# Kernel optimization log

Measured on AMD Instinct MI355X. Metric: run time of the kernel, lower is better.

## Reference

```python
import jax, jax.numpy as jnp
import numpy as np

B, S, D, H = 2, 2048, 2048, 16
HD = D // H


def setup_inputs() -> dict:
    key = jax.random.key(0)
    kx, = jax.random.split(key, 1)
    return {
        "x": jax.random.normal(kx, (B, S, D), dtype=jnp.float32),
        "q_mask": jnp.ones((D, D), dtype=jnp.float32),
        "k_mask": jnp.ones((D, D), dtype=jnp.float32),
        "v_mask": jnp.ones((D, D), dtype=jnp.float32),
        "out_mask": jnp.ones((D, D), dtype=jnp.float32),
        "head_mask": jnp.ones((H,), dtype=jnp.float32),
        "attention_mask": jnp.ones((B, S), dtype=jnp.float32),
        "shared_weight": jnp.float32(1.0),
    }


def reference(x, q_mask, k_mask, v_mask, out_mask, head_mask, attention_mask, shared_weight):
    b, s, d = x.shape
    scale = jnp.float32(HD) ** -0.5

    def shared_linear(inp, mask):
        # F.linear(x, mask * shared_weight): out = inp @ (mask*sw).T
        return jnp.einsum("bsd,ed->bse", inp, mask * shared_weight)

    q = shared_linear(x, q_mask).reshape(b, s, H, HD).transpose(0, 2, 1, 3)  # [B,H,S,HD]
    k = shared_linear(x, k_mask).reshape(b, s, H, HD).transpose(0, 2, 1, 3)
    v = shared_linear(x, v_mask).reshape(b, s, H, HD).transpose(0, 2, 1, 3)

    hm = head_mask.reshape(1, H, 1, 1)
    q, k, v = q * hm, k * hm, v * hm

    scores = jnp.einsum("bhqd,bhkd->bhqk", q, k) * scale  # [B,H,S,S]

    # causal mask: upper triangle (j > i) -> -inf
    causal = jnp.triu(jnp.ones((s, s), dtype=bool), k=1)
    scores = jnp.where(causal, -jnp.inf, scores)

    # additive attention mask: (1 - m) * -10000, broadcast [B,1,1,S]
    scores = scores + (1.0 - attention_mask)[:, None, None, :] * -10000.0

    attn = jax.nn.softmax(scores, axis=-1)  # dropout is identity in eval / p=0

    out = jnp.einsum("bhqk,bhkd->bhqd", attn, v)          # [B,H,S,HD]
    out = out.transpose(0, 2, 1, 3).reshape(b, s, d)       # [B,S,D]
    return shared_linear(out, out_mask)
```

## Files before the change

kernel.cpp:

```cpp
#include <hip/hip_runtime.h>

#define B_  2
#define S_  2048
#define D_  2048
#define H_  16
#define HD_ 128

typedef __bf16 bf16;
typedef __bf16 bf16x4 __attribute__((ext_vector_type(4)));
typedef __bf16 bf16x8 __attribute__((ext_vector_type(8)));
typedef float  f32x4  __attribute__((ext_vector_type(4)));

__device__ __forceinline__ void gld_lds16(const void* g, void* l) {
    __builtin_amdgcn_global_load_lds(
        (const __attribute__((address_space(1))) unsigned int*)g,
        (__attribute__((address_space(3))) unsigned int*)l, 16, 0, 0);
}

__global__ __launch_bounds__(256)
void precast_kernel(const float* __restrict__ x, bf16* __restrict__ xh,
                    bf16* __restrict__ xl) {
    int i = (blockIdx.x * 256 + threadIdx.x) * 8;
    float4 a = *(const float4*)(x + i);
    float4 b = *(const float4*)(x + i + 4);
    float av[8] = {a.x, a.y, a.z, a.w, b.x, b.y, b.z, b.w};
    bf16x8 h8, l8;
#pragma unroll
    for (int e = 0; e < 8; e++) {
        bf16 hv = (bf16)av[e];
        h8[e] = hv;
        l8[e] = (bf16)(av[e] - (float)hv);
    }
    *(bf16x8*)(xh + i) = h8;
    *(bf16x8*)(xl + i) = l8;
}

__global__ __launch_bounds__(256)
void transpose_v(const bf16* __restrict__ vp, bf16* __restrict__ vt) {
    const int bh = blockIdx.x >> 5;
    const int s0 = (blockIdx.x & 31) * 64;
    const int t = threadIdx.x;
    __shared__ bf16 tile[128 * 72];
    const bf16* src = vp + (size_t)bh * S_ * HD_;
    bf16* dst = vt + (size_t)bh * HD_ * S_;

    {
        int r = t >> 2;
        int g = (t & 3) * 4;
#pragma unroll
        for (int w = 0; w < 4; w++) {
            bf16x8 v8 = *(const bf16x8*)&src[(size_t)(s0 + r) * HD_ + (g + w) * 8];
#pragma unroll
            for (int e = 0; e < 8; e++) tile[((g + w) * 8 + e) * 72 + r] = v8[e];
        }
    }
    __syncthreads();
    {
        int d = t >> 1;
        int sg0 = (t & 1) * 4;
#pragma unroll
        for (int w = 0; w < 4; w++) {
            int sg = sg0 + w;
            *(bf16x8*)&dst[(size_t)d * S_ + s0 + sg * 8] =
                *(const bf16x8*)&tile[d * 72 + sg * 8];
        }
    }
}

#define BK 64

template<int MODE>
__global__ __launch_bounds__(256, 3)
void gemm_nt(const bf16* __restrict__ Ah_g, const bf16* __restrict__ Al_g,
             const float* __restrict__ B0, const float* __restrict__ B1,
             const float* __restrict__ B2,
             const float* __restrict__ swp, const float* __restrict__ hm,
             bf16* __restrict__ qh_, bf16* __restrict__ ql_,
             bf16* __restrict__ kh_, bf16* __restrict__ kl_,
             bf16* __restrict__ vp_, float* __restrict__ Cf) {
    const int K = D_;
    __shared__ bf16 Ah[128 * 64];
    __shared__ bf16 Al[128 * 64];
    __shared__ bf16 Bs[128 * 64];
    const int t = threadIdx.x;
    const int wave = t >> 6, lane = t & 63;
    const int wr = wave >> 1, wc = wave & 1;
    const int m0 = blockIdx.y * 128, n0 = blockIdx.x * 128;
    const int lrow = lane & 15, lquad = lane >> 4;
    const float sw = swp[0];

    const int which = (MODE == 0) ? (n0 >> 11) : 0;
    const bool split = (MODE == 0) && (which < 2);

    const float* Bp;
    if (MODE == 0) {
        Bp = (which == 0) ? B0 : ((which == 1) ? B1 : B2);
        Bp += (size_t)(n0 & (D_ - 1)) * K;
    } else {
        Bp = B0 + (size_t)n0 * K;
    }

    const int srow8 = lane >> 3;
    const int sgrp  = lane & 7;
    const int g0 = (lquad)     ^ (lrow & 7);
    const int g1 = (lquad + 4) ^ (lrow & 7);

    f32x4 acc[4][4];
#pragma unroll
    for (int i = 0; i < 4; i++)
#pragma unroll
        for (int j = 0; j < 4; j++) acc[i][j] = (f32x4){0.f, 0.f, 0.f, 0.f};

    for (int k0 = 0; k0 < K; k0 += BK) {
#pragma unroll
        for (int p = 0; p < 4; p++) {
            int r = wave * 32 + p * 8 + srow8;
            int gcol = (sgrp ^ (r & 7)) * 8;
            gld_lds16(Ah_g + (size_t)(m0 + r) * K + k0 + gcol,
                      &Ah[(wave * 32 + p * 8) * 64]);
            if (split)
                gld_lds16(Al_g + (size_t)(m0 + r) * K + k0 + gcol,
                          &Al[(wave * 32 + p * 8) * 64]);
        }
#pragma unroll
        for (int p = 0; p < 4; p++) {
            int r = p * 32 + (t >> 3);
            int gcol = (sgrp ^ (r & 7)) * 8;
            const float* bp = Bp + (size_t)r * K + k0 + gcol;
            float4 blo = *(const float4*)bp;
            float4 bhi = *(const float4*)(bp + 4);
            bf16x8 b8;
            b8[0] = (bf16)(blo.x * sw); b8[1] = (bf16)(blo.y * sw);
            b8[2] = (bf16)(blo.z * sw); b8[3] = (bf16)(blo.w * sw);
            b8[4] = (bf16)(bhi.x * sw); b8[5] = (bf16)(bhi.y * sw);
            b8[6] = (bf16)(bhi.z * sw); b8[7] = (bf16)(bhi.w * sw);
            *(bf16x8*)&Bs[r * 64 + sgrp * 8] = b8;
        }
        __syncthreads();

#pragma unroll
        for (int kk = 0; kk < 2; kk++) {
            const int gA = kk ? g1 : g0;
            bf16x8 afh[4], afl[4], bfr[4];
#pragma unroll
            for (int i = 0; i < 4; i++) {
                int row = wr * 64 + i * 16 + lrow;
                afh[i] = *(const bf16x8*)&Ah[row * 64 + gA * 8];
                if (split) afl[i] = *(const bf16x8*)&Al[row * 64 + gA * 8];
            }
#pragma unroll
            for (int j = 0; j < 4; j++) {
                int row = wc * 64 + j * 16 + lrow;
                bfr[j] = *(const bf16x8*)&Bs[row * 64 + gA * 8];
            }
#pragma unroll
            for (int i = 0; i < 4; i++)
#pragma unroll
                for (int j = 0; j < 4; j++) {
                    acc[i][j] = __builtin_amdgcn_mfma_f32_16x16x32_bf16(
                        afh[i], bfr[j], acc[i][j], 0, 0, 0);
                    if (split)
                        acc[i][j] = __builtin_amdgcn_mfma_f32_16x16x32_bf16(
                            afl[i], bfr[j], acc[i][j], 0, 0, 0);
                }
        }
        __syncthreads();
    }

#pragma unroll
    for (int i = 0; i < 4; i++) {
#pragma unroll
        for (int j = 0; j < 4; j++) {
#pragma unroll
            for (int r = 0; r < 4; r++) {
                int m = m0 + wr * 64 + i * 16 + lquad * 4 + r;
                int n = n0 + wc * 64 + j * 16 + lrow;
                float v = acc[i][j][r];
                if (MODE == 0) {
                    int e = n & (D_ - 1);
                    int h = e >> 7, hd = e & (HD_ - 1);
                    int b = m >> 11, s = m & (S_ - 1);
                    v *= hm[h];
                    size_t idx = (((size_t)b * H_ + h) * S_ + s) * HD_ + hd;
                    if (which == 2) {
                        vp_[idx] = (bf16)v;
                    } else {
                        bf16 hv = (bf16)v;
                        bf16 lv = (bf16)(v - (float)hv);
                        if (which == 0) { qh_[idx] = hv; ql_[idx] = lv; }
                        else            { kh_[idx] = hv; kl_[idx] = lv; }
                    }
                } else {
                    Cf[(size_t)m * D_ + n] = v;
                }
            }
        }
    }
}

#define SPLD 72

__global__ __launch_bounds__(256, 2)
void attn_kernel(const bf16* __restrict__ qh_, const bf16* __restrict__ ql_,
                 const bf16* __restrict__ kh_, const bf16* __restrict__ kl_,
                 const bf16* __restrict__ vt_, const float* __restrict__ am,
                 bf16* __restrict__ outp) {
    const int bh = blockIdx.x & 31;
    const int qblk = 31 - (blockIdx.x >> 5);
    const int b = bh >> 4, h = bh & 15;
    const int i0 = qblk * 64;
    const int t = threadIdx.x, wave = t >> 6, lane = t & 63;
    const int lrow = lane & 15, quad = lane >> 4;

    __shared__ bf16 skh[64 * 128];
    __shared__ bf16 skl[64 * 128];
    __shared__ bf16 svt[128 * 64];
    __shared__ bf16 sp[4][16 * SPLD];

    const size_t kbase = (size_t)bh * S_ * HD_;
    const size_t vbase = (size_t)bh * HD_ * S_;

    const int qrow = i0 + wave * 16 + lrow;
    bf16x8 qhf[4], qlf[4];
#pragma unroll
    for (int c = 0; c < 4; c++) {
        qhf[c] = *(const bf16x8*)&qh_[kbase + (size_t)qrow * HD_ + c * 32 + quad * 8];
        qlf[c] = *(const bf16x8*)&ql_[kbase + (size_t)qrow * HD_ + c * 32 + quad * 8];
    }

    float m_i[4], l_i[4];
    f32x4 O[8];
#pragma unroll
    for (int r = 0; r < 4; r++) { m_i[r] = -INFINITY; l_i[r] = 0.f; }
#pragma unroll
    for (int n2 = 0; n2 < 8; n2++) O[n2] = (f32x4){0.f, 0.f, 0.f, 0.f};

    const float scale = 0.08838834764831845f;

    for (int j0 = 0; j0 <= i0; j0 += 64) {
        __syncthreads();
#pragma unroll
        for (int p = 0; p < 4; p++) {
            int rb = wave * 16 + p * 4;
            int r = rb + (lane >> 4);
            int gl = ((lane & 15) ^ (r & 7)) * 8;
            gld_lds16(kh_ + kbase + (size_t)(j0 + r) * HD_ + gl, &skh[rb * 128]);
            gld_lds16(kl_ + kbase + (size_t)(j0 + r) * HD_ + gl, &skl[rb * 128]);
        }
#pragma unroll
        for (int p = 0; p < 4; p++) {
            int db = wave * 32 + p * 8;
            int d = db + (lane >> 3);
            int gl = ((lane & 7) ^ (d & 7)) * 8;
            gld_lds16(vt_ + vbase + (size_t)d * S_ + j0 + gl, &svt[db * 64]);
        }
        __syncthreads();

        float amadd[4];
#pragma unroll
        for (int nt = 0; nt < 4; nt++)
            amadd[nt] = (1.0f - am[b * S_ + j0 + nt * 16 + lrow]) * -10000.0f;

        f32x4 s4[4];
#pragma unroll
        for (int nt = 0; nt < 4; nt++) s4[nt] = (f32x4){0.f, 0.f, 0.f, 0.f};
#pragma unroll
        for (int c = 0; c < 4; c++) {
#pragma unroll
            for (int nt = 0; nt < 4; nt++) {
                int ka = (nt * 16 + lrow) * 128 + (((c * 4 + quad) ^ (lrow & 7)) * 8);
                bf16x8 kb8 = *(const bf16x8*)&skh[ka];
                bf16x8 lb8 = *(const bf16x8*)&skl[ka];
                s4[nt] = __builtin_amdgcn_mfma_f32_16x16x32_bf16(qhf[c], kb8, s4[nt], 0, 0, 0);
                s4[nt] = __builtin_amdgcn_mfma_f32_16x16x32_bf16(qhf[c], lb8, s4[nt], 0, 0, 0);
                s4[nt] = __builtin_amdgcn_mfma_f32_16x16x32_bf16(qlf[c], kb8, s4[nt], 0, 0, 0);
            }
        }

        const bool diag = (j0 == i0);
#pragma unroll
        for (int r = 0; r < 4; r++) {
            const int rrow = wave * 16 + quad * 4 + r;
            float sv[4], pw[4];
            float mx = -INFINITY;
#pragma unroll
            for (int nt = 0; nt < 4; nt++) {
                float xv = s4[nt][r] * scale + amadd[nt];
                if (diag && (nt * 16 + lrow) > rrow) xv = -INFINITY;
                sv[nt] = xv;
                mx = fmaxf(mx, xv);
            }
#pragma unroll
            for (int off = 1; off < 16; off <<= 1) mx = fmaxf(mx, __shfl_xor(mx, off));
            float mnew = fmaxf(m_i[r], mx);
            float alpha = __expf(m_i[r] - mnew);
            float ps = 0.f;
#pragma unroll
            for (int nt = 0; nt < 4; nt++) { pw[nt] = __expf(sv[nt] - mnew); ps += pw[nt]; }
#pragma unroll
            for (int off = 1; off < 16; off <<= 1) ps += __shfl_xor(ps, off);
            l_i[r] = l_i[r] * alpha + ps;
            m_i[r] = mnew;
#pragma unroll
            for (int n2 = 0; n2 < 8; n2++) O[n2][r] *= alpha;
#pragma unroll
            for (int nt = 0; nt < 4; nt++)
                sp[wave][(quad * 4 + r) * SPLD + nt * 16 + lrow] = (bf16)pw[nt];
        }
        __asm__ volatile("s_waitcnt lgkmcnt(0)" ::: "memory");

#pragma unroll
        for (int k2 = 0; k2 < 2; k2++) {
            bf16x8 pf = *(const bf16x8*)&sp[wave][lrow * SPLD + k2 * 32 + quad * 8];
            const int gp = ((quad + k2 * 4) ^ (lrow & 7)) * 8;
#pragma unroll
            for (int n2 = 0; n2 < 8; n2++) {
                bf16x8 vf8 = *(const bf16x8*)&svt[(n2 * 16 + lrow) * 64 + gp];
                O[n2] = __builtin_amdgcn_mfma_f32_16x16x32_bf16(pf, vf8, O[n2], 0, 0, 0);
            }
        }
    }

    float inv[4];
#pragma unroll
    for (int r = 0; r < 4; r++) inv[r] = 1.0f / l_i[r];
#pragma unroll
    for (int n2 = 0; n2 < 8; n2++)
#pragma unroll
        for (int r = 0; r < 4; r++) {
            int srow = i0 + wave * 16 + quad * 4 + r;
            outp[((size_t)(b * S_ + srow)) * D_ + h * HD_ + n2 * 16 + lrow] =
                (bf16)(O[n2][r] * inv[r]);
        }
}

extern "C" void kernel_launch(void* const* d_in, const int* in_sizes, int n_in,
                              void* d_out, int out_size, void* d_ws, size_t ws_size,
                              hipStream_t stream) {
    const float* x  = (const float*)d_in[0];
    const float* qm = (const float*)d_in[1];
    const float* km = (const float*)d_in[2];
    const float* vm = (const float*)d_in[3];
    const float* om = (const float*)d_in[4];
    const float* hm = (const float*)d_in[5];
    const float* am = (const float*)d_in[6];
    const float* sw = (const float*)d_in[7];
    float* out = (float*)d_out;

    const size_t P = (size_t)B_ * H_ * S_ * HD_ * sizeof(bf16);
    char* ws = (char*)d_ws;
    bf16* xh = (bf16*)(ws + 0 * P);
    bf16* xl = (bf16*)(ws + 1 * P);
    bf16* qh = (bf16*)(ws + 2 * P);
    bf16* ql = (bf16*)(ws + 3 * P);
    bf16* kh = (bf16*)(ws + 4 * P);
    bf16* kl = (bf16*)(ws + 5 * P);
    bf16* vp = (bf16*)d_out;
    bf16* vt = (bf16*)((char*)d_out + P);
    bf16* attn_out = (bf16*)(ws + 0 * P);

    precast_kernel<<<(B_ * S_ * D_) / (256 * 8), 256, 0, stream>>>(x, xh, xl);

    gemm_nt<0><<<dim3(48, 32), 256, 0, stream>>>(
        xh, xl, qm, km, vm, sw, hm, qh, ql, kh, kl, vp, nullptr);

    transpose_v<<<1024, 256, 0, stream>>>(vp, vt);

    attn_kernel<<<1024, 256, 0, stream>>>(qh, ql, kh, kl, vt, am, attn_out);

    gemm_nt<1><<<dim3(16, 32), 256, 0, stream>>>(
        attn_out, nullptr, om, nullptr, nullptr, sw, hm,
        nullptr, nullptr, nullptr, nullptr, nullptr, out);
}
```

Baseline: 493.7 us.

## Double-buffer 32-key attention tiles with prefetch and per-wave causal skipping

The attention loop now works on 32-key chunks held in double-buffered LDS, issuing async global-to-LDS loads for the next chunk before computing the current one, so only one barrier is needed per iteration. Each wave skips chunks lying entirely above its own causal diagonal. The row-sum of probabilities moves from a shuffle reduction to an extra MFMA against a ones vector. LDS drops to one shared buffer and launch bounds rise to 3 blocks per CU for occupancy, at the cost of more loop iterations and a tighter register budget.

Measured after the change: 496.7 us. No clear change (+0.6%).

```diff
diff --git a/kernel.cpp b/kernel.cpp
--- a/kernel.cpp
+++ b/kernel.cpp
@@ -43,7 +43,6 @@
     __shared__ bf16 tile[128 * 72];
     const bf16* src = vp + (size_t)bh * S_ * HD_;
     bf16* dst = vt + (size_t)bh * HD_ * S_;
-
     {
         int r = t >> 2;
         int g = (t & 3) * 4;
@@ -198,9 +197,7 @@
     }
 }
 
-#define SPLD 72
-
-__global__ __launch_bounds__(256, 2)
+__global__ __launch_bounds__(256, 3)
 void attn_kernel(const bf16* __restrict__ qh_, const bf16* __restrict__ ql_,
                  const bf16* __restrict__ kh_, const bf16* __restrict__ kl_,
                  const bf16* __restrict__ vt_, const float* __restrict__ am,
@@ -212,10 +209,11 @@
     const int t = threadIdx.x, wave = t >> 6, lane = t & 63;
     const int lrow = lane & 15, quad = lane >> 4;
 
-    __shared__ bf16 skh[64 * 128];
-    __shared__ bf16 skl[64 * 128];
-    __shared__ bf16 svt[128 * 64];
-    __shared__ bf16 sp[4][16 * SPLD];
+    __shared__ bf16 sh[26624];
+    bf16* skh = sh;
+    bf16* skl = sh + 8192;
+    bf16* svt = sh + 16384;
+    bf16* sp  = sh + 24576 + wave * 512;
 
     const size_t kbase = (size_t)bh * S_ * HD_;
     const size_t vbase = (size_t)bh * HD_ * S_;
@@ -228,102 +226,130 @@
         qlf[c] = *(const bf16x8*)&ql_[kbase + (size_t)qrow * HD_ + c * 32 + quad * 8];
     }
 
-    float m_i[4], l_i[4];
-    f32x4 O[8];
-#pragma unroll
-    for (int r = 0; r < 4; r++) { m_i[r] = -INFINITY; l_i[r] = 0.f; }
+    bf16x8 ones8;
+#pragma unroll
+    for (int e = 0; e < 8; e++) ones8[e] = (bf16)1.0f;
+
+    float m_i[4];
+    f32x4 O[8], Ol;
+#pragma unroll
+    for (int r = 0; r < 4; r++) m_i[r] = -INFINITY;
 #pragma unroll
     for (int n2 = 0; n2 < 8; n2++) O[n2] = (f32x4){0.f, 0.f, 0.f, 0.f};
+    Ol = (f32x4){0.f, 0.f, 0.f, 0.f};
 
     const float scale = 0.08838834764831845f;
-
-    for (int j0 = 0; j0 <= i0; j0 += 64) {
+    const int iwmin = i0 + wave * 16;
+    const int iwmax = iwmin + 15;
+    const int nch = (i0 + 64) >> 5;
+
+    {
+#pragma unroll
+        for (int p = 0; p < 2; p++) {
+            int rb = wave * 8 + p * 4;
+            int r  = rb + (lane >> 4);
+            int gl = ((lane & 15) ^ (r & 7)) * 8;
+            gld_lds16(kh_ + kbase + (size_t)r * HD_ + gl, skh + rb * 128);
+            gld_lds16(kl_ + kbase + (size_t)r * HD_ + gl, skl + rb * 128);
+        }
+#pragma unroll
+        for (int p = 0; p < 2; p++) {
+            int db = wave * 32 + p * 16;
+            int d  = db + (lane >> 2);
+            int gl = ((lane & 3) ^ (d & 3)) * 8;
+            gld_lds16(vt_ + vbase + (size_t)d * S_ + gl, svt + db * 32);
+        }
+    }
+
+    for (int c = 0; c < nch; c++) {
         __syncthreads();
-#pragma unroll
-        for (int p = 0; p < 4; p++) {
-            int rb = wave * 16 + p * 4;
-            int r = rb + (lane >> 4);
-            int gl = ((lane & 15) ^ (r & 7)) * 8;
-            gld_lds16(kh_ + kbase + (size_t)(j0 + r) * HD_ + gl, &skh[rb * 128]);
-            gld_lds16(kl_ + kbase + (size_t)(j0 + r) * HD_ + gl, &skl[rb * 128]);
-        }
-#pragma unroll
-        for (int p = 0; p < 4; p++) {
-            int db = wave * 32 + p * 8;
-            int d = db + (lane >> 3);
-            int gl = ((lane & 7) ^ (d & 7)) * 8;
-            gld_lds16(vt_ + vbase + (size_t)d * S_ + j0 + gl, &svt[db * 64]);
-        }
-        __syncthreads();
-
-        float amadd[4];
-#pragma unroll
-        for (int nt = 0; nt < 4; nt++)
-            amadd[nt] = (1.0f - am[b * S_ + j0 + nt * 16 + lrow]) * -10000.0f;
-
-        f32x4 s4[4];
-#pragma unroll
-        for (int nt = 0; nt < 4; nt++) s4[nt] = (f32x4){0.f, 0.f, 0.f, 0.f};
-#pragma unroll
-        for (int c = 0; c < 4; c++) {
-#pragma unroll
-            for (int nt = 0; nt < 4; nt++) {
-                int ka = (nt * 16 + lrow) * 128 + (((c * 4 + quad) ^ (lrow & 7)) * 8);
-                bf16x8 kb8 = *(const bf16x8*)&skh[ka];
-                bf16x8 lb8 = *(const bf16x8*)&skl[ka];
-                s4[nt] = __builtin_amdgcn_mfma_f32_16x16x32_bf16(qhf[c], kb8, s4[nt], 0, 0, 0);
-                s4[nt] = __builtin_amdgcn_mfma_f32_16x16x32_bf16(qhf[c], lb8, s4[nt], 0, 0, 0);
-                s4[nt] = __builtin_amdgcn_mfma_f32_16x16x32_bf16(qlf[c], kb8, s4[nt], 0, 0, 0);
-            }
-        }
-
-        const bool diag = (j0 == i0);
+        if (c + 1 < nch) {
+            const int j0s = (c + 1) * 32;
+            bf16* dkh = skh + ((c + 1) & 1) * 4096;
+            bf16* dkl = skl + ((c + 1) & 1) * 4096;
+            bf16* dvt = svt + ((c + 1) & 1) * 4096;
+#pragma unroll
+            for (int p = 0; p < 2; p++) {
+                int rb = wave * 8 + p * 4;
+                int r  = rb + (lane >> 4);
+                int gl = ((lane & 15) ^ (r & 7)) * 8;
+                gld_lds16(kh_ + kbase + (size_t)(j0s + r) * HD_ + gl, dkh + rb * 128);
+                gld_lds16(kl_ + kbase + (size_t)(j0s + r) * HD_ + gl, dkl + rb * 128);
+            }
+#pragma unroll
+            for (int p = 0; p < 2; p++) {
+                int db = wave * 32 + p * 16;
+                int d  = db + (lane >> 2);
+                int gl = ((lane & 3) ^ (d & 3)) * 8;
+                gld_lds16(vt_ + vbase + (size_t)d * S_ + j0s + gl, dvt + db * 32);
+            }
+        }
+
+        const int j0 = c * 32;
+        if (j0 > iwmax) continue;
+
+        const bf16* kH = skh + (c & 1) * 4096;
+        const bf16* kL = skl + (c & 1) * 4096;
+        const bf16* vT = svt + (c & 1) * 4096;
+
+        float amadd0 = (1.0f - am[b * S_ + j0 + lrow])      * -10000.0f;
+        float amadd1 = (1.0f - am[b * S_ + j0 + 16 + lrow]) * -10000.0f;
+
+        f32x4 s4[2];
+        s4[0] = (f32x4){0.f, 0.f, 0.f, 0.f};
+        s4[1] = (f32x4){0.f, 0.f, 0.f, 0.f};
+#pragma unroll
+        for (int cg = 0; cg < 4; cg++) {
+#pragma unroll
+            for (int nt = 0; nt < 2; nt++) {
+                int ka = (nt * 16 + lrow) * 128 + (((cg * 4 + quad) ^ (lrow & 7)) * 8);
+                bf16x8 kb8 = *(const bf16x8*)&kH[ka];
+                bf16x8 lb8 = *(const bf16x8*)&kL[ka];
+                s4[nt] = __builtin_amdgcn_mfma_f32_16x16x32_bf16(qhf[cg], kb8, s4[nt], 0, 0, 0);
+                s4[nt] = __builtin_amdgcn_mfma_f32_16x16x32_bf16(qhf[cg], lb8, s4[nt], 0, 0, 0);
+                s4[nt] = __builtin_amdgcn_mfma_f32_16x16x32_bf16(qlf[cg], kb8, s4[nt], 0, 0, 0);
+            }
+        }
+
+        const bool msk = (j0 + 31 > iwmin);
 #pragma unroll
         for (int r = 0; r < 4; r++) {
-            const int rrow = wave * 16 + quad * 4 + r;
-            float sv[4], pw[4];
-            float mx = -INFINITY;
-#pragma unroll
-            for (int nt = 0; nt < 4; nt++) {
-                float xv = s4[nt][r] * scale + amadd[nt];
-                if (diag && (nt * 16 + lrow) > rrow) xv = -INFINITY;
-                sv[nt] = xv;
-                mx = fmaxf(mx, xv);
-            }
+            const int irow = iwmin + quad * 4 + r;
+            float x0 = s4[0][r] * scale + amadd0;
+            float x1 = s4[1][r] * scale + amadd1;
+            if (msk) {
+                if (j0 + lrow > irow)      x0 = -INFINITY;
+                if (j0 + 16 + lrow > irow) x1 = -INFINITY;
+            }
+            float mx = fmaxf(x0, x1);
 #pragma unroll
             for (int off = 1; off < 16; off <<= 1) mx = fmaxf(mx, __shfl_xor(mx, off));
             float mnew = fmaxf(m_i[r], mx);
             float alpha = __expf(m_i[r] - mnew);
-            float ps = 0.f;
-#pragma unroll
-            for (int nt = 0; nt < 4; nt++) { pw[nt] = __expf(sv[nt] - mnew); ps += pw[nt]; }
-#pragma unroll
-            for (int off = 1; off < 16; off <<= 1) ps += __shfl_xor(ps, off);
-            l_i[r] = l_i[r] * alpha + ps;
             m_i[r] = mnew;
+            float p0 = __expf(x0 - mnew);
+            float p1 = __expf(x1 - mnew);
+            Ol[r] *= alpha;
 #pragma unroll
             for (int n2 = 0; n2 < 8; n2++) O[n2][r] *= alpha;
-#pragma unroll
-            for (int nt = 0; nt < 4; nt++)
-                sp[wave][(quad * 4 + r) * SPLD + nt * 16 + lrow] = (bf16)pw[nt];
+            const int rl = quad * 4 + r;
+            sp[rl * 32 + (((lrow >> 3) ^ (rl & 3)) * 8) + (lrow & 7)] = (bf16)p0;
+            sp[rl * 32 + ((((lrow >> 3) + 2) ^ (rl & 3)) * 8) + (lrow & 7)] = (bf16)p1;
         }
         __asm__ volatile("s_waitcnt lgkmcnt(0)" ::: "memory");
 
-#pragma unroll
-        for (int k2 = 0; k2 < 2; k2++) {
-            bf16x8 pf = *(const bf16x8*)&sp[wave][lrow * SPLD + k2 * 32 + quad * 8];
-            const int gp = ((quad + k2 * 4) ^ (lrow & 7)) * 8;
-#pragma unroll
-            for (int n2 = 0; n2 < 8; n2++) {
-                bf16x8 vf8 = *(const bf16x8*)&svt[(n2 * 16 + lrow) * 64 + gp];
-                O[n2] = __builtin_amdgcn_mfma_f32_16x16x32_bf16(pf, vf8, O[n2], 0, 0, 0);
-            }
-        }
+        bf16x8 pf = *(const bf16x8*)&sp[lrow * 32 + ((quad ^ (lrow & 3)) * 8)];
+#pragma unroll
+        for (int n2 = 0; n2 < 8; n2++) {
+            bf16x8 vf8 = *(const bf16x8*)&vT[(n2 * 16 + lrow) * 32 + ((quad ^ (lrow & 3)) * 8)];
+            O[n2] = __builtin_amdgcn_mfma_f32_16x16x32_bf16(pf, vf8, O[n2], 0, 0, 0);
+        }
+        Ol = __builtin_amdgcn_mfma_f32_16x16x32_bf16(pf, ones8, Ol, 0, 0, 0);
     }
 
     float inv[4];
 #pragma unroll
-    for (int r = 0; r < 4; r++) inv[r] = 1.0f / l_i[r];
+    for (int r = 0; r < 4; r++) inv[r] = 1.0f / Ol[r];
 #pragma unroll
     for (int n2 = 0; n2 < 8; n2++)
 #pragma unroll
```

## Register-prefetch K/V tiles, use exp2 softmax, compute row sums via MFMA

Applied to the files above, without the earlier changes.

Replaces the direct global-to-LDS loads with register prefetching of the next K/V chunk, which overlaps global loads with the current chunk's compute. Switches the softmax to exp2 with the log2e factor folded into the scale and the mask constant. Drops the shuffle-based row-sum reduction and instead accumulates the row sum with an extra MFMA against a vector of ones. This trades higher register pressure and an extra LDS store pass for less shuffle and latency cost, and the row sum is now taken from the bf16-rounded probabilities.

Result: no change. 495.7 us (+0.4%).

```diff
diff --git a/kernel.cpp b/kernel.cpp
--- a/kernel.cpp
+++ b/kernel.cpp
@@ -43,7 +43,6 @@
     __shared__ bf16 tile[128 * 72];
     const bf16* src = vp + (size_t)bh * S_ * HD_;
     bf16* dst = vt + (size_t)bh * HD_ * S_;
-
     {
         int r = t >> 2;
         int g = (t & 3) * 4;
@@ -220,6 +219,23 @@
     const size_t kbase = (size_t)bh * S_ * HD_;
     const size_t vbase = (size_t)bh * HD_ * S_;
 
+    int krr[4], kcc[4], ldk[4];
+#pragma unroll
+    for (int p = 0; p < 4; p++) {
+        int r = wave * 16 + p * 4 + (lane >> 4);
+        krr[p] = r;
+        kcc[p] = ((lane & 15) ^ (r & 7)) * 8;
+        ldk[p] = r * 128 + (lane & 15) * 8;
+    }
+    int vdd[4], vcc[4], ldv[4];
+#pragma unroll
+    for (int p = 0; p < 4; p++) {
+        int d = wave * 32 + p * 8 + (lane >> 3);
+        vdd[p] = d;
+        vcc[p] = ((lane & 7) ^ (d & 7)) * 8;
+        ldv[p] = d * 64 + (lane & 7) * 8;
+    }
+
     const int qrow = i0 + wave * 16 + lrow;
     bf16x8 qhf[4], qlf[4];
 #pragma unroll
@@ -228,52 +244,67 @@
         qlf[c] = *(const bf16x8*)&ql_[kbase + (size_t)qrow * HD_ + c * 32 + quad * 8];
     }
 
-    float m_i[4], l_i[4];
-    f32x4 O[8];
-#pragma unroll
-    for (int r = 0; r < 4; r++) { m_i[r] = -INFINITY; l_i[r] = 0.f; }
+    bf16x8 ones8;
+#pragma unroll
+    for (int e = 0; e < 8; e++) ones8[e] = (bf16)1.0f;
+
+    float m_i[4];
+    f32x4 O[8], Ol;
+#pragma unroll
+    for (int r = 0; r < 4; r++) m_i[r] = -INFINITY;
 #pragma unroll
     for (int n2 = 0; n2 < 8; n2++) O[n2] = (f32x4){0.f, 0.f, 0.f, 0.f};
-
-    const float scale = 0.08838834764831845f;
-
-    for (int j0 = 0; j0 <= i0; j0 += 64) {
+    Ol = (f32x4){0.f, 0.f, 0.f, 0.f};
+
+    const float scale2 = 0.08838834764831845f * 1.44269504088896f;
+    const int nch = (i0 >> 6) + 1;
+
+    bf16x8 pkh[4], pkl[4], pvt[4];
+#pragma unroll
+    for (int p = 0; p < 4; p++) {
+        pkh[p] = *(const bf16x8*)&kh_[kbase + (size_t)krr[p] * HD_ + kcc[p]];
+        pkl[p] = *(const bf16x8*)&kl_[kbase + (size_t)krr[p] * HD_ + kcc[p]];
+        pvt[p] = *(const bf16x8*)&vt_[vbase + (size_t)vdd[p] * S_ + vcc[p]];
+    }
+
+    for (int c = 0; c < nch; c++) {
+        const int j0 = c * 64;
         __syncthreads();
 #pragma unroll
         for (int p = 0; p < 4; p++) {
-            int rb = wave * 16 + p * 4;
-            int r = rb + (lane >> 4);
-            int gl = ((lane & 15) ^ (r & 7)) * 8;
-            gld_lds16(kh_ + kbase + (size_t)(j0 + r) * HD_ + gl, &skh[rb * 128]);
-            gld_lds16(kl_ + kbase + (size_t)(j0 + r) * HD_ + gl, &skl[rb * 128]);
-        }
-#pragma unroll
-        for (int p = 0; p < 4; p++) {
-            int db = wave * 32 + p * 8;
-            int d = db + (lane >> 3);
-            int gl = ((lane & 7) ^ (d & 7)) * 8;
-            gld_lds16(vt_ + vbase + (size_t)d * S_ + j0 + gl, &svt[db * 64]);
+            *(bf16x8*)&skh[ldk[p]] = pkh[p];
+            *(bf16x8*)&skl[ldk[p]] = pkl[p];
+            *(bf16x8*)&svt[ldv[p]] = pvt[p];
         }
         __syncthreads();
+        if (c + 1 < nch) {
+            const int j0n = j0 + 64;
+#pragma unroll
+            for (int p = 0; p < 4; p++) {
+                pkh[p] = *(const bf16x8*)&kh_[kbase + (size_t)(j0n + krr[p]) * HD_ + kcc[p]];
+                pkl[p] = *(const bf16x8*)&kl_[kbase + (size_t)(j0n + krr[p]) * HD_ + kcc[p]];
+                pvt[p] = *(const bf16x8*)&vt_[vbase + (size_t)vdd[p] * S_ + j0n + vcc[p]];
+            }
+        }
 
         float amadd[4];
 #pragma unroll
         for (int nt = 0; nt < 4; nt++)
-            amadd[nt] = (1.0f - am[b * S_ + j0 + nt * 16 + lrow]) * -10000.0f;
+            amadd[nt] = (1.0f - am[b * S_ + j0 + nt * 16 + lrow]) * -14426.950408f;
 
         f32x4 s4[4];
 #pragma unroll
         for (int nt = 0; nt < 4; nt++) s4[nt] = (f32x4){0.f, 0.f, 0.f, 0.f};
 #pragma unroll
-        for (int c = 0; c < 4; c++) {
+        for (int cg = 0; cg < 4; cg++) {
 #pragma unroll
             for (int nt = 0; nt < 4; nt++) {
-                int ka = (nt * 16 + lrow) * 128 + (((c * 4 + quad) ^ (lrow & 7)) * 8);
+                int ka = (nt * 16 + lrow) * 128 + (((cg * 4 + quad) ^ (lrow & 7)) * 8);
                 bf16x8 kb8 = *(const bf16x8*)&skh[ka];
                 bf16x8 lb8 = *(const bf16x8*)&skl[ka];
-                s4[nt] = __builtin_amdgcn_mfma_f32_16x16x32_bf16(qhf[c], kb8, s4[nt], 0, 0, 0);
-                s4[nt] = __builtin_amdgcn_mfma_f32_16x16x32_bf16(qhf[c], lb8, s4[nt], 0, 0, 0);
-                s4[nt] = __builtin_amdgcn_mfma_f32_16x16x32_bf16(qlf[c], kb8, s4[nt], 0, 0, 0);
+                s4[nt] = __builtin_amdgcn_mfma_f32_16x16x32_bf16(qhf[cg], kb8, s4[nt], 0, 0, 0);
+                s4[nt] = __builtin_amdgcn_mfma_f32_16x16x32_bf16(qhf[cg], lb8, s4[nt], 0, 0, 0);
+                s4[nt] = __builtin_amdgcn_mfma_f32_16x16x32_bf16(qlf[cg], kb8, s4[nt], 0, 0, 0);
             }
         }
 
@@ -281,11 +312,11 @@
 #pragma unroll
         for (int r = 0; r < 4; r++) {
             const int rrow = wave * 16 + quad * 4 + r;
-            float sv[4], pw[4];
+            float sv[4];
             float mx = -INFINITY;
 #pragma unroll
             for (int nt = 0; nt < 4; nt++) {
-                float xv = s4[nt][r] * scale + amadd[nt];
+                float xv = s4[nt][r] * scale2 + amadd[nt];
                 if (diag && (nt * 16 + lrow) > rrow) xv = -INFINITY;
                 sv[nt] = xv;
                 mx = fmaxf(mx, xv);
@@ -293,19 +324,14 @@
 #pragma unroll
             for (int off = 1; off < 16; off <<= 1) mx = fmaxf(mx, __shfl_xor(mx, off));
             float mnew = fmaxf(m_i[r], mx);
-            float alpha = __expf(m_i[r] - mnew);
-            float ps = 0.f;
-#pragma unroll
-            for (int nt = 0; nt < 4; nt++) { pw[nt] = __expf(sv[nt] - mnew); ps += pw[nt]; }
-#pragma unroll
-            for (int off = 1; off < 16; off <<= 1) ps += __shfl_xor(ps, off);
-            l_i[r] = l_i[r] * alpha + ps;
+            float alpha = exp2f(m_i[r] - mnew);
             m_i[r] = mnew;
+            Ol[r] *= alpha;
 #pragma unroll
             for (int n2 = 0; n2 < 8; n2++) O[n2][r] *= alpha;
 #pragma unroll
             for (int nt = 0; nt < 4; nt++)
-                sp[wave][(quad * 4 + r) * SPLD + nt * 16 + lrow] = (bf16)pw[nt];
+                sp[wave][(quad * 4 + r) * SPLD + nt * 16 + lrow] = (bf16)exp2f(sv[nt] - mnew);
         }
         __asm__ volatile("s_waitcnt lgkmcnt(0)" ::: "memory");
 
@@ -318,12 +344,13 @@
                 bf16x8 vf8 = *(const bf16x8*)&svt[(n2 * 16 + lrow) * 64 + gp];
                 O[n2] = __builtin_amdgcn_mfma_f32_16x16x32_bf16(pf, vf8, O[n2], 0, 0, 0);
             }
+            Ol = __builtin_amdgcn_mfma_f32_16x16x32_bf16(pf, ones8, Ol, 0, 0, 0);
         }
     }
 
     float inv[4];
 #pragma unroll
-    for (int r = 0; r < 4; r++) inv[r] = 1.0f / l_i[r];
+    for (int r = 0; r < 4; r++) inv[r] = 1.0f / Ol[r];
 #pragma unroll
     for (int n2 = 0; n2 < 8; n2++)
 #pragma unroll
```
